# Kernel tuning notes

Hardware: AMD Instinct MI355X
Metric: run time of the kernel (lower is better)

Reference implementation:

```python
import jax, jax.numpy as jnp
import numpy as np

EPS = 1e-5
C_M, C, C_Z = 256, 32, 128
N_SEQ, N_RES = 256, 1024


def setup_inputs() -> dict:
    key = jax.random.key(0)
    k1, k2, k3 = jax.random.split(key, 3)
    msa = jax.random.normal(k1, (N_SEQ, N_RES, C_M), dtype=jnp.float32)
    norm_w = jnp.ones((C_M,), dtype=jnp.float32)
    norm_b = jnp.zeros((C_M,), dtype=jnp.float32)
    w_ab = jax.random.normal(k2, (C, C_M), dtype=jnp.float32) * (1.0 / np.sqrt(C_M))
    b_ab = jnp.zeros((C,), dtype=jnp.float32)
    w_out = jax.random.normal(k3, (C_Z, C * C), dtype=jnp.float32) * (1.0 / C)
    b_out = jnp.zeros((C_Z,), dtype=jnp.float32)
    return {"msa": msa, "norm_w": norm_w, "norm_b": norm_b,
            "w_ab": w_ab, "b_ab": b_ab, "w_out": w_out, "b_out": b_out}


def reference(msa, norm_w, norm_b, w_ab, b_ab, w_out, b_out):
    # msa: (s, r, c_m) -> (r, s, c_m)
    x = jnp.transpose(msa, (1, 0, 2))
    s = x.shape[1]
    # LayerNorm over c_m
    mu = jnp.mean(x, axis=-1, keepdims=True)
    var = jnp.mean(jnp.square(x - mu), axis=-1, keepdims=True)
    xn = (x - mu) * jax.lax.rsqrt(var + EPS) * norm_w + norm_b
    # a == b: same linear applied twice to same input in the original
    a = jnp.einsum('rsm,cm->rsc', xn, w_ab) + b_ab          # (r, s, c)
    # mean over s of outer product == batched A^T A / s  -> (r, c, c)
    o = jnp.einsum('rsx,rsy->rxy', a, a) / s
    o = o.reshape(o.shape[0], C * C)                        # (r, c*c)
    pre_pair = jnp.einsum('rk,zk->rz', o, w_out) + b_out    # (r, c_z)
    r = pre_pair.shape[0]
    # unsqueeze(1).expand(r, r, c_z)
    pair = jnp.broadcast_to(pre_pair[:, None, :], (r, r, C_Z))
    return pair
```

## Files before the change

kernel.cpp:

```cpp
#include <hip/hip_runtime.h>

#define NSEQ 256
#define NRES 1024
#define CM   256
#define CC   32
#define CZ   128
#define EPS  1e-5f
#define SROW (NRES * CM)
#define MCH  32
#define XPAD 36

typedef float f4v __attribute__((ext_vector_type(4)));

__launch_bounds__(256, 2)
__global__ void opm_stage1(const float* __restrict__ msa,
                           const float* __restrict__ nw,
                           const float* __restrict__ nb,
                           const float* __restrict__ w_ab,
                           const float* __restrict__ b_ab,
                           const float* __restrict__ w_out,
                           const float* __restrict__ b_out,
                           float* __restrict__ pre)
{
    __shared__ float wt[CM * CC];
    __shared__ float xt[NSEQ * XPAD];
    __shared__ float o_lds[CC * CC];
    __shared__ float K1p[8 * CC], K2p[8 * CC];
    __shared__ float K1[CC], K2[CC];
    __shared__ float pre_part[2 * CZ];
    __shared__ float pre_lds[CZ];

    const int tid = threadIdx.x;
    const int r   = blockIdx.x;

    {
        const int c  = tid & 31;
        const int m0 = tid >> 5;
        #pragma unroll
        for (int k = 0; k < 32; ++k) {
            const int m = m0 + (k << 3);
            wt[m * CC + c] = nw[m] * w_ab[c * CM + m];
        }
    }
    __syncthreads();
    {
        const int c    = tid & 31;
        const int part = tid >> 5;
        float k1 = 0.f, k2 = 0.f;
        #pragma unroll 8
        for (int i = 0; i < 32; ++i) {
            const int m = part * 32 + i;
            k1 += wt[m * CC + c];
            k2 = fmaf(nb[m], w_ab[c * CM + m], k2);
        }
        K1p[part * CC + c] = k1;
        K2p[part * CC + c] = k2;
    }
    __syncthreads();
    if (tid < CC) {
        float k1 = 0.f, k2 = 0.f;
        #pragma unroll
        for (int p = 0; p < 8; ++p) { k1 += K1p[p * CC + tid]; k2 += K2p[p * CC + tid]; }
        K1[tid] = k1;
        K2[tid] = k2 + b_ab[tid];
    }

    const int sc = tid & 7;
    const int sg = tid >> 3;
    const int c0 = sc * 4;
    const float* xr = msa + (size_t)r * CM;

    float G[8][4];
    float ssum[8], ssq[8];
    #pragma unroll
    for (int j = 0; j < 8; ++j) {
        ssum[j] = 0.f; ssq[j] = 0.f;
        #pragma unroll
        for (int cc = 0; cc < 4; ++cc) G[j][cc] = 0.f;
    }

    float4 pf[8];
    #pragma unroll
    for (int k = 0; k < 8; ++k)
        pf[k] = *(const float4*)(xr + (size_t)(sg + (k << 5)) * SROW + (sc << 2));

    for (int mb = 0; mb < CM; mb += MCH) {
        __syncthreads();
        #pragma unroll
        for (int k = 0; k < 8; ++k)
            *(float4*)&xt[(sg + (k << 5)) * XPAD + (sc << 2)] = pf[k];
        __syncthreads();
        if (mb + MCH < CM) {
            #pragma unroll
            for (int k = 0; k < 8; ++k)
                pf[k] = *(const float4*)(xr + (size_t)(sg + (k << 5)) * SROW + (mb + MCH) + (sc << 2));
        }
        #pragma unroll
        for (int mm = 0; mm < MCH; mm += 4) {
            const float4 w0 = *(const float4*)&wt[(mb + mm + 0) * CC + c0];
            const float4 w1 = *(const float4*)&wt[(mb + mm + 1) * CC + c0];
            const float4 w2 = *(const float4*)&wt[(mb + mm + 2) * CC + c0];
            const float4 w3 = *(const float4*)&wt[(mb + mm + 3) * CC + c0];
            #pragma unroll
            for (int j = 0; j < 8; ++j) {
                const float4 x4 = *(const float4*)&xt[(sg + (j << 5)) * XPAD + mm];
                G[j][0] = fmaf(x4.x, w0.x, fmaf(x4.y, w1.x, fmaf(x4.z, w2.x, fmaf(x4.w, w3.x, G[j][0]))));
                G[j][1] = fmaf(x4.x, w0.y, fmaf(x4.y, w1.y, fmaf(x4.z, w2.y, fmaf(x4.w, w3.y, G[j][1]))));
                G[j][2] = fmaf(x4.x, w0.z, fmaf(x4.y, w1.z, fmaf(x4.z, w2.z, fmaf(x4.w, w3.z, G[j][2]))));
                G[j][3] = fmaf(x4.x, w0.w, fmaf(x4.y, w1.w, fmaf(x4.z, w2.w, fmaf(x4.w, w3.w, G[j][3]))));
                ssum[j] += (x4.x + x4.y) + (x4.z + x4.w);
                ssq[j]  = fmaf(x4.x, x4.x, fmaf(x4.y, x4.y, fmaf(x4.z, x4.z, fmaf(x4.w, x4.w, ssq[j]))));
            }
        }
    }

    float a_reg[8][4];
    {
        const float k1a = K1[c0 + 0], k1b = K1[c0 + 1], k1c = K1[c0 + 2], k1d = K1[c0 + 3];
        const float k2a = K2[c0 + 0], k2b = K2[c0 + 1], k2c = K2[c0 + 2], k2d = K2[c0 + 3];
        #pragma unroll
        for (int j = 0; j < 8; ++j) {
            const float mu   = ssum[j] * (1.f / CM);
            const float var  = ssq[j] * (1.f / CM) - mu * mu;
            const float rstd = 1.f / sqrtf(var + EPS);
            a_reg[j][0] = fmaf(rstd, G[j][0] - mu * k1a, k2a);
            a_reg[j][1] = fmaf(rstd, G[j][1] - mu * k1b, k2b);
            a_reg[j][2] = fmaf(rstd, G[j][2] - mu * k1c, k2c);
            a_reg[j][3] = fmaf(rstd, G[j][3] - mu * k1d, k2d);
        }
    }
    __syncthreads();
    #pragma unroll
    for (int j = 0; j < 8; ++j) {
        const int s = sg + (j << 5);
        *(float4*)&xt[s * CC + c0] =
            make_float4(a_reg[j][0], a_reg[j][1], a_reg[j][2], a_reg[j][3]);
    }
    __syncthreads();

    const int xi = (tid >> 4) << 1;
    const int yi = (tid & 15) << 1;
    float o00 = 0.f, o01 = 0.f, o10 = 0.f, o11 = 0.f;
    #pragma unroll 4
    for (int s = 0; s < NSEQ; ++s) {
        const float2 ax = *(const float2*)&xt[s * CC + xi];
        const float2 ay = *(const float2*)&xt[s * CC + yi];
        o00 = fmaf(ax.x, ay.x, o00);
        o01 = fmaf(ax.x, ay.y, o01);
        o10 = fmaf(ax.y, ay.x, o10);
        o11 = fmaf(ax.y, ay.y, o11);
    }
    {
        const float inv_s = 1.f / NSEQ;
        *(float2*)&o_lds[xi * CC + yi]       = make_float2(o00 * inv_s, o01 * inv_s);
        *(float2*)&o_lds[(xi + 1) * CC + yi] = make_float2(o10 * inv_s, o11 * inv_s);
    }
    __syncthreads();

    {
        const int z    = tid & 127;
        const int half = tid >> 7;
        const float* wrow = w_out + (size_t)z * (CC * CC) + half * 512;
        const float* op   = o_lds + half * 512;
        float po = 0.f;
        #pragma unroll 8
        for (int k = 0; k < 512; k += 4) {
            const float4 o4 = *(const float4*)&op[k];
            const float4 w4 = *(const float4*)&wrow[k];
            po = fmaf(o4.x, w4.x, fmaf(o4.y, w4.y, fmaf(o4.z, w4.z, fmaf(o4.w, w4.w, po))));
        }
        pre_part[half * CZ + z] = po;
    }
    __syncthreads();
    if (tid < CZ) pre_lds[tid] = pre_part[tid] + pre_part[CZ + tid] + b_out[tid];
    __syncthreads();

    if (tid < 32) {
        ((float4*)pre)[(size_t)r * 32 + tid] = *(const float4*)&pre_lds[tid * 4];
    }
}

__launch_bounds__(256, 8)
__global__ void opm_bcast(const float* __restrict__ pre,
                          float* __restrict__ out)
{
    const int tid = threadIdx.x;
    const size_t chunk = (size_t)blockIdx.x * 16384;
    const int r = (int)(chunk >> 15);
    const f4v pv = ((const f4v*)pre)[(r << 5) + (tid & 31)];
    f4v* op = (f4v*)out + chunk + tid;
    #pragma unroll 8
    for (int k = 0; k < 64; ++k)
        __builtin_nontemporal_store(pv, op + (size_t)k * 256);
}

extern "C" void kernel_launch(void* const* d_in, const int* in_sizes, int n_in,
                              void* d_out, int out_size, void* d_ws, size_t ws_size,
                              hipStream_t stream) {
    const float* msa   = (const float*)d_in[0];
    const float* nw    = (const float*)d_in[1];
    const float* nb    = (const float*)d_in[2];
    const float* w_ab  = (const float*)d_in[3];
    const float* b_ab  = (const float*)d_in[4];
    const float* w_out = (const float*)d_in[5];
    const float* b_out = (const float*)d_in[6];
    float* out = (float*)d_out;
    float* pre = (float*)d_ws;

    opm_stage1<<<NRES, 256, 0, stream>>>(msa, nw, nb, w_ab, b_ab, w_out, b_out, pre);
    opm_bcast<<<2048, 256, 0, stream>>>(pre, out);
}
```

Before: 892.8 us.

## Split fused OPM kernel into prep, coalesced LayerNorm-linear, and Gram stages

Replaces the single per-residue kernel with four stages. A one-block prep kernel folds the norm weight into the projection weights once. An LN+linear kernel then reads msa rows in contiguous per-(s,r) order, where the old kernel used strided gathers across sequences. It writes the projected activations to a workspace, and a separate Gram kernel reads them back per residue. This trades strided msa reads and redundant per-block weight prep for an extra 32 MB workspace round trip and extra launches, and it also switches the broadcast stores from nontemporal to normal.

```diff
diff --git a/kernel.cpp b/kernel.cpp
--- a/kernel.cpp
+++ b/kernel.cpp
@@ -6,69 +6,68 @@
 #define CC   32
 #define CZ   128
 #define EPS  1e-5f
-#define SROW (NRES * CM)
-#define MCH  32
-#define XPAD 36
+#define MCH  16
+#define XTS  20
+#define ASS  34
 
 typedef float f4v __attribute__((ext_vector_type(4)));
 
-__launch_bounds__(256, 2)
-__global__ void opm_stage1(const float* __restrict__ msa,
-                           const float* __restrict__ nw,
-                           const float* __restrict__ nb,
-                           const float* __restrict__ w_ab,
-                           const float* __restrict__ b_ab,
-                           const float* __restrict__ w_out,
-                           const float* __restrict__ b_out,
-                           float* __restrict__ pre)
+__launch_bounds__(256, 1)
+__global__ void opm_prep(const float* __restrict__ nw, const float* __restrict__ nb,
+                         const float* __restrict__ w_ab, const float* __restrict__ b_ab,
+                         float* __restrict__ wt_g, float* __restrict__ k12_g)
+{
+    __shared__ float wt_s[CM * CC];
+    const int m = threadIdx.x;
+    const float nwm = nw[m];
+    #pragma unroll 8
+    for (int c = 0; c < CC; ++c)
+        wt_s[m * CC + c] = nwm * w_ab[c * CM + m];
+    __syncthreads();
+    #pragma unroll
+    for (int k = 0; k < 8; ++k)
+        ((f4v*)wt_g)[m * 8 + k] = *(const f4v*)&wt_s[m * CC + k * 4];
+    if (m < CC) {
+        float k1 = 0.f, k2 = 0.f;
+        for (int mm = 0; mm < CM; ++mm) {
+            k1 += wt_s[mm * CC + m];
+            k2 = fmaf(nb[mm], w_ab[m * CM + mm], k2);
+        }
+        k12_g[m]      = k1;
+        k12_g[CC + m] = k2 + b_ab[m];
+    }
+}
+
+__launch_bounds__(256, 3)
+__global__ void opm_ln_lin(const float* __restrict__ msa,
+                           const float* __restrict__ wt_g,
+                           const float* __restrict__ k12_g,
+                           float* __restrict__ a_g)
 {
     __shared__ float wt[CM * CC];
-    __shared__ float xt[NSEQ * XPAD];
-    __shared__ float o_lds[CC * CC];
-    __shared__ float K1p[8 * CC], K2p[8 * CC];
-    __shared__ float K1[CC], K2[CC];
-    __shared__ float pre_part[2 * CZ];
-    __shared__ float pre_lds[CZ];
+    __shared__ float xt[256 * XTS];
+    __shared__ float K1c[CC], K2c[CC];
 
     const int tid = threadIdx.x;
-    const int r   = blockIdx.x;
-
-    {
-        const int c  = tid & 31;
-        const int m0 = tid >> 5;
-        #pragma unroll
-        for (int k = 0; k < 32; ++k) {
-            const int m = m0 + (k << 3);
-            wt[m * CC + c] = nw[m] * w_ab[c * CM + m];
-        }
-    }
-    __syncthreads();
-    {
-        const int c    = tid & 31;
-        const int part = tid >> 5;
-        float k1 = 0.f, k2 = 0.f;
-        #pragma unroll 8
-        for (int i = 0; i < 32; ++i) {
-            const int m = part * 32 + i;
-            k1 += wt[m * CC + c];
-            k2 = fmaf(nb[m], w_ab[c * CM + m], k2);
-        }
-        K1p[part * CC + c] = k1;
-        K2p[part * CC + c] = k2;
-    }
-    __syncthreads();
-    if (tid < CC) {
-        float k1 = 0.f, k2 = 0.f;
-        #pragma unroll
-        for (int p = 0; p < 8; ++p) { k1 += K1p[p * CC + tid]; k2 += K2p[p * CC + tid]; }
-        K1[tid] = k1;
-        K2[tid] = k2 + b_ab[tid];
-    }
+    const int s   = blockIdx.x >> 2;
+    const int r0  = (blockIdx.x & 3) << 8;
+
+    {
+        const f4v* src = (const f4v*)wt_g;
+        #pragma unroll
+        for (int k = 0; k < 8; ++k)
+            ((f4v*)wt)[tid + (k << 8)] = src[tid + (k << 8)];
+        if (tid < CC) { K1c[tid] = k12_g[tid]; K2c[tid] = k12_g[CC + tid]; }
+    }
+
+    const float* xrow = msa + ((size_t)s * NRES + r0 + tid) * CM;
+    float4 pf[4];
+    #pragma unroll
+    for (int k = 0; k < 4; ++k) pf[k] = *(const float4*)(xrow + (k << 2));
 
     const int sc = tid & 7;
     const int sg = tid >> 3;
-    const int c0 = sc * 4;
-    const float* xr = msa + (size_t)r * CM;
+    const int c0 = sc << 2;
 
     float G[8][4];
     float ssum[8], ssq[8];
@@ -78,22 +77,17 @@
         #pragma unroll
         for (int cc = 0; cc < 4; ++cc) G[j][cc] = 0.f;
     }
-
-    float4 pf[8];
-    #pragma unroll
-    for (int k = 0; k < 8; ++k)
-        pf[k] = *(const float4*)(xr + (size_t)(sg + (k << 5)) * SROW + (sc << 2));
+    __syncthreads();
 
     for (int mb = 0; mb < CM; mb += MCH) {
-        __syncthreads();
-        #pragma unroll
-        for (int k = 0; k < 8; ++k)
-            *(float4*)&xt[(sg + (k << 5)) * XPAD + (sc << 2)] = pf[k];
+        #pragma unroll
+        for (int k = 0; k < 4; ++k)
+            *(float4*)&xt[tid * XTS + (k << 2)] = pf[k];
         __syncthreads();
         if (mb + MCH < CM) {
             #pragma unroll
-            for (int k = 0; k < 8; ++k)
-                pf[k] = *(const float4*)(xr + (size_t)(sg + (k << 5)) * SROW + (mb + MCH) + (sc << 2));
+            for (int k = 0; k < 4; ++k)
+                pf[k] = *(const float4*)(xrow + mb + MCH + (k << 2));
         }
         #pragma unroll
         for (int mm = 0; mm < MCH; mm += 4) {
@@ -103,7 +97,7 @@
             const float4 w3 = *(const float4*)&wt[(mb + mm + 3) * CC + c0];
             #pragma unroll
             for (int j = 0; j < 8; ++j) {
-                const float4 x4 = *(const float4*)&xt[(sg + (j << 5)) * XPAD + mm];
+                const float4 x4 = *(const float4*)&xt[(sg + (j << 5)) * XTS + mm];
                 G[j][0] = fmaf(x4.x, w0.x, fmaf(x4.y, w1.x, fmaf(x4.z, w2.x, fmaf(x4.w, w3.x, G[j][0]))));
                 G[j][1] = fmaf(x4.x, w0.y, fmaf(x4.y, w1.y, fmaf(x4.z, w2.y, fmaf(x4.w, w3.y, G[j][1]))));
                 G[j][2] = fmaf(x4.x, w0.z, fmaf(x4.y, w1.z, fmaf(x4.z, w2.z, fmaf(x4.w, w3.z, G[j][2]))));
@@ -112,29 +106,47 @@
                 ssq[j]  = fmaf(x4.x, x4.x, fmaf(x4.y, x4.y, fmaf(x4.z, x4.z, fmaf(x4.w, x4.w, ssq[j]))));
             }
         }
-    }
-
-    float a_reg[8][4];
-    {
-        const float k1a = K1[c0 + 0], k1b = K1[c0 + 1], k1c = K1[c0 + 2], k1d = K1[c0 + 3];
-        const float k2a = K2[c0 + 0], k2b = K2[c0 + 1], k2c = K2[c0 + 2], k2d = K2[c0 + 3];
+        __syncthreads();
+    }
+
+    {
+        const float k1a = K1c[c0 + 0], k1b = K1c[c0 + 1], k1c = K1c[c0 + 2], k1d = K1c[c0 + 3];
+        const float k2a = K2c[c0 + 0], k2b = K2c[c0 + 1], k2c = K2c[c0 + 2], k2d = K2c[c0 + 3];
         #pragma unroll
         for (int j = 0; j < 8; ++j) {
             const float mu   = ssum[j] * (1.f / CM);
             const float var  = ssq[j] * (1.f / CM) - mu * mu;
             const float rstd = 1.f / sqrtf(var + EPS);
-            a_reg[j][0] = fmaf(rstd, G[j][0] - mu * k1a, k2a);
-            a_reg[j][1] = fmaf(rstd, G[j][1] - mu * k1b, k2b);
-            a_reg[j][2] = fmaf(rstd, G[j][2] - mu * k1c, k2c);
-            a_reg[j][3] = fmaf(rstd, G[j][3] - mu * k1d, k2d);
-        }
-    }
-    __syncthreads();
-    #pragma unroll
-    for (int j = 0; j < 8; ++j) {
-        const int s = sg + (j << 5);
-        *(float4*)&xt[s * CC + c0] =
-            make_float4(a_reg[j][0], a_reg[j][1], a_reg[j][2], a_reg[j][3]);
+            f4v av;
+            av.x = fmaf(rstd, G[j][0] - mu * k1a, k2a);
+            av.y = fmaf(rstd, G[j][1] - mu * k1b, k2b);
+            av.z = fmaf(rstd, G[j][2] - mu * k1c, k2c);
+            av.w = fmaf(rstd, G[j][3] - mu * k1d, k2d);
+            const size_t row = (size_t)s * NRES + r0 + sg + (j << 5);
+            *(f4v*)&a_g[row * CC + c0] = av;
+        }
+    }
+}
+
+__launch_bounds__(256, 4)
+__global__ void opm_gram(const float* __restrict__ a_g,
+                         const float* __restrict__ w_out,
+                         const float* __restrict__ b_out,
+                         float* __restrict__ pre)
+{
+    __shared__ float as[NSEQ * ASS];
+    __shared__ float o_lds[CC * CC];
+    __shared__ float pre_part[2 * CZ];
+    __shared__ float pre_lds[CZ];
+
+    const int tid = threadIdx.x;
+    const int r   = blockIdx.x;
+
+    {
+        const f4v* src = (const f4v*)(a_g + ((size_t)tid * NRES + r) * CC);
+        #pragma unroll
+        for (int k = 0; k < 8; ++k)
+            *(f4v*)&as[tid * ASS + (k << 2)] = src[k];
     }
     __syncthreads();
 
@@ -143,8 +155,8 @@
     float o00 = 0.f, o01 = 0.f, o10 = 0.f, o11 = 0.f;
     #pragma unroll 4
     for (int s = 0; s < NSEQ; ++s) {
-        const float2 ax = *(const float2*)&xt[s * CC + xi];
-        const float2 ay = *(const float2*)&xt[s * CC + yi];
+        const float2 ax = *(const float2*)&as[s * ASS + xi];
+        const float2 ay = *(const float2*)&as[s * ASS + yi];
         o00 = fmaf(ax.x, ay.x, o00);
         o01 = fmaf(ax.x, ay.y, o01);
         o10 = fmaf(ax.y, ay.x, o10);
@@ -174,10 +186,8 @@
     __syncthreads();
     if (tid < CZ) pre_lds[tid] = pre_part[tid] + pre_part[CZ + tid] + b_out[tid];
     __syncthreads();
-
-    if (tid < 32) {
-        ((float4*)pre)[(size_t)r * 32 + tid] = *(const float4*)&pre_lds[tid * 4];
-    }
+    if (tid < 32)
+        ((f4v*)pre)[(size_t)r * 32 + tid] = *(const f4v*)&pre_lds[tid * 4];
 }
 
 __launch_bounds__(256, 8)
@@ -186,12 +196,12 @@
 {
     const int tid = threadIdx.x;
     const size_t chunk = (size_t)blockIdx.x * 16384;
-    const int r = (int)(chunk >> 15);
+    const int r = blockIdx.x >> 1;
     const f4v pv = ((const f4v*)pre)[(r << 5) + (tid & 31)];
     f4v* op = (f4v*)out + chunk + tid;
     #pragma unroll 8
     for (int k = 0; k < 64; ++k)
-        __builtin_nontemporal_store(pv, op + (size_t)k * 256);
+        op[(size_t)k * 256] = pv;
 }
 
 extern "C" void kernel_launch(void* const* d_in, const int* in_sizes, int n_in,
@@ -205,8 +215,15 @@
     const float* w_out = (const float*)d_in[5];
     const float* b_out = (const float*)d_in[6];
     float* out = (float*)d_out;
-    float* pre = (float*)d_ws;
-
-    opm_stage1<<<NRES, 256, 0, stream>>>(msa, nw, nb, w_ab, b_ab, w_out, b_out, pre);
+
+    float* ws   = (float*)d_ws;
+    float* a_g  = ws;
+    float* pre  = ws + (size_t)NSEQ * NRES * CC;
+    float* wt_g = pre + (size_t)NRES * CZ;
+    float* k12  = wt_g + CM * CC;
+
+    opm_prep<<<1, 256, 0, stream>>>(nw, nb, w_ab, b_ab, wt_g, k12);
+    opm_ln_lin<<<NSEQ * 4, 256, 0, stream>>>(msa, wt_g, k12, a_g);
+    opm_gram<<<NRES, 256, 0, stream>>>(a_g, w_out, b_out, pre);
     opm_bcast<<<2048, 256, 0, stream>>>(pre, out);
 }
```

Result: no change. 885.8 us (-0.8%).
